# Kernel optimization log

Measured on AMD Instinct MI355X. Metric: run time of the kernel, lower is better.

The kernel has to match this reference:

```python
import math
import jax, jax.numpy as jnp
import numpy as np

HEADS = 8
D_MODEL = 256


def positional_encoding_2d(c, h, w):
    # faithful port of wzlxjtu/PositionalEncoding2D
    d = c // 2
    div_term = jnp.exp(jnp.arange(0.0, d, 2, dtype=jnp.float32) * (-(math.log(10000.0) / d)))  # [d//2? no: d/2 entries -> d//2]
    pos_w = jnp.arange(0.0, w, dtype=jnp.float32)[:, None] * div_term  # [w, d//2]
    pos_h = jnp.arange(0.0, h, dtype=jnp.float32)[:, None] * div_term  # [h, d//2]
    pe = jnp.zeros((c, h, w), dtype=jnp.float32)
    sw = jnp.broadcast_to(jnp.sin(pos_w).T[:, None, :], (div_term.shape[0], h, w))
    cw = jnp.broadcast_to(jnp.cos(pos_w).T[:, None, :], (div_term.shape[0], h, w))
    sh = jnp.broadcast_to(jnp.sin(pos_h).T[:, :, None], (div_term.shape[0], h, w))
    ch = jnp.broadcast_to(jnp.cos(pos_h).T[:, :, None], (div_term.shape[0], h, w))
    pe = pe.at[0:d:2].set(sw)
    pe = pe.at[1:d:2].set(cw)
    pe = pe.at[d::2].set(sh)
    pe = pe.at[d + 1::2].set(ch)
    return pe


def setup_inputs() -> dict:
    key = jax.random.key(0)
    ks = jax.random.split(key, 9)
    b, c, h, w = 2, D_MODEL, 64, 64
    x = jax.random.normal(ks[0], (b, c, h, w), dtype=jnp.float32)
    s = 0.02
    Wq = jax.random.normal(ks[1], (c, c), dtype=jnp.float32) * s
    Wk = jax.random.normal(ks[2], (c, c), dtype=jnp.float32) * s
    Wv = jax.random.normal(ks[3], (c, c), dtype=jnp.float32) * s
    Wo = jax.random.normal(ks[4], (c, c), dtype=jnp.float32) * s
    bq = jax.random.normal(ks[5], (c,), dtype=jnp.float32) * s
    bk = jax.random.normal(ks[6], (c,), dtype=jnp.float32) * s
    bv = jax.random.normal(ks[7], (c,), dtype=jnp.float32) * s
    bo = jax.random.normal(ks[8], (c,), dtype=jnp.float32) * s
    return {"x": x, "Wq": Wq, "bq": bq, "Wk": Wk, "bk": bk,
            "Wv": Wv, "bv": bv, "Wo": Wo, "bo": bo}


def reference(x, Wq, bq, Wk, bk, Wv, bv, Wo, bo):
    b, c, h, w = x.shape
    dk = c // HEADS
    pe = positional_encoding_2d(c, h, w)
    x2 = x + pe[None]                                   # [b,c,h,w]
    tok = x2.reshape(b, c, h * w).transpose(0, 2, 1)    # [b,N,c]
    q = (tok @ Wq.T + bq).reshape(b, -1, HEADS, dk).transpose(0, 2, 1, 3)  # [b,H,N,dk]
    k = (tok @ Wk.T + bk).reshape(b, -1, HEADS, dk).transpose(0, 2, 1, 3)
    v = (tok @ Wv.T + bv).reshape(b, -1, HEADS, dk).transpose(0, 2, 1, 3)
    scores = jnp.einsum('bhnd,bhmd->bhnm', q, k) / math.sqrt(dk)  # [b,H,N,N]
    attn = jax.nn.softmax(scores, axis=-1)
    out = jnp.einsum('bhnm,bhmd->bhnd', attn, v)        # [b,H,N,dk]
    concat = out.transpose(0, 2, 1, 3).reshape(b, -1, c)  # [b,N,c]
    proj = concat @ Wo.T + bo                           # [b,N,c]
    return proj.transpose(0, 2, 1).reshape(b, c, h, w)
```

## Files before the change

kernel.cpp:

```cpp
#include <hip/hip_runtime.h>
#include <hip/hip_bf16.h>
#include <cstdint>

typedef float f32x4 __attribute__((ext_vector_type(4)));
typedef __bf16 bf16x8 __attribute__((ext_vector_type(8)));
typedef uint32_t uint2v __attribute__((ext_vector_type(2)));

#define MFMA_K32(A, B, C) __builtin_amdgcn_mfma_f32_16x16x32_bf16((A), (B), (C), 0, 0, 0)

#if __has_builtin(__builtin_amdgcn_exp2f)
#define EXP2(x) __builtin_amdgcn_exp2f(x)
#else
#define EXP2(x) exp2f(x)
#endif

static __device__ __forceinline__ uint16_t f2b(float f) {
    uint32_t u = __float_as_uint(f);
    uint32_t r = (u + 0x7fffu + ((u >> 16) & 1u)) >> 16;
    return (uint16_t)r;
}

static __device__ __forceinline__ uint32_t packbf(float a, float b) {
    uint32_t r;
    asm("v_cvt_pk_bf16_f32 %0, %1, %2" : "=v"(r) : "v"(a), "v"(b));
    return r;
}

__global__ __launch_bounds__(512) void prep(const float* __restrict__ x,
                                            const float* __restrict__ wq,
                                            const float* __restrict__ wk,
                                            const float* __restrict__ wv,
                                            const float* __restrict__ wo,
                                            uint16_t* __restrict__ dst,
                                            uint16_t* __restrict__ tok) {
    __shared__ uint16_t T[64][65];
    int tid = threadIdx.x, bid = blockIdx.x;
    if (bid < 512) {
        int nt = bid & 63, ct = (bid >> 6) & 3, bb = bid >> 8;
        int n0 = nt << 6, c0 = ct << 6;
        int nl = tid & 63, cq = tid >> 6;
        int n = n0 + nl;
        float pf = (float)((c0 & 128) ? nt : nl);
        int cbase = c0 + cq * 8;
        int ibase = (cbase & 127) >> 1;
        float dt = __expf((float)(2 * ibase) * -0.07195578415606394f);
#pragma unroll
        for (int j = 0; j < 4; ++j) {
            float sv, cv;
            __sincosf(pf * dt, &sv, &cv);
            int cl = cq * 8 + 2 * j;
            int cc = cbase + 2 * j;
            T[cl][nl]     = f2b(x[((size_t)(bb * 256 + cc) << 12) + n] + sv);
            T[cl + 1][nl] = f2b(x[((size_t)(bb * 256 + cc + 1) << 12) + n] + cv);
            dt *= 0.8659643233600653f;
        }
        __syncthreads();
#pragma unroll
        for (int p = 0; p < 8; ++p) {
            int tl = cq * 8 + p;
            tok[(((size_t)(bb << 12) | (n0 + tl)) << 8) + c0 + nl] = T[nl][tl];
        }
    } else {
        int idx = (bid - 512) * 512 + tid;
        int which = idx >> 16, off = idx & 65535;
        const float* s = (which == 0) ? wq : (which == 1) ? wk : (which == 2) ? wv : wo;
        dst[idx] = f2b(s[off]);
    }
}

__global__ __launch_bounds__(256) void qkv_gemm(const uint16_t* __restrict__ tok,
                                                const uint16_t* __restrict__ Wall,
                                                const float* __restrict__ bq,
                                                const float* __restrict__ bk,
                                                const float* __restrict__ bv,
                                                uint16_t* __restrict__ qo,
                                                uint16_t* __restrict__ ko,
                                                uint16_t* __restrict__ vo) {
    __shared__ __align__(16) uint16_t WS[64][264];
    int tid = threadIdx.x, wv = tid >> 6, lane = tid & 63;
    int c16 = lane & 15, quad = lane >> 4;
    int M0 = blockIdx.x * 64 + wv * 16;
    int O0 = blockIdx.y * 64;
    const uint16_t* arow = tok + (size_t)(M0 + c16) * 256;
    bf16x8 af[8];
#pragma unroll
    for (int kk = 0; kk < 8; ++kk) af[kk] = *(const bf16x8*)(arow + kk * 32 + quad * 8);
    f32x4 zero = {0.f, 0.f, 0.f, 0.f};
    int bb = M0 >> 12, n = (M0 + c16) & 4095;
    int srow = tid >> 5, sch = (tid & 31) << 3;
    for (int mat = 0; mat < 3; ++mat) {
        const uint16_t* Wg = Wall + (size_t)mat * 65536 + (size_t)O0 * 256;
        __syncthreads();
#pragma unroll
        for (int p = 0; p < 8; ++p)
            *(bf16x8*)(&WS[p * 8 + srow][sch]) = *(const bf16x8*)(Wg + (p * 8 + srow) * 256 + sch);
        __syncthreads();
        f32x4 acc[4] = {zero, zero, zero, zero};
#pragma unroll
        for (int kk = 0; kk < 8; ++kk) {
            int k0 = kk * 32 + quad * 8;
#pragma unroll
            for (int nb = 0; nb < 4; ++nb)
                acc[nb] = MFMA_K32(*(const bf16x8*)(&WS[nb * 16 + c16][k0]),
                                   af[kk], acc[nb]);
        }
        const float* bias = (mat == 0) ? bq : (mat == 1) ? bk : bv;
        if (mat < 2) {
            float scale = (mat == 0) ? 0.25505654134660127f : 1.0f;
            uint16_t* dst = (mat == 0) ? qo : ko;
#pragma unroll
            for (int nb = 0; nb < 4; ++nb) {
                int o = O0 + nb * 16 + quad * 4;
                f32x4 bi = *(const f32x4*)(bias + o);
                int h = o >> 5, dd = o & 31;
                uint2v pk;
                pk[0] = packbf((acc[nb][0] + bi[0]) * scale, (acc[nb][1] + bi[1]) * scale);
                pk[1] = packbf((acc[nb][2] + bi[2]) * scale, (acc[nb][3] + bi[3]) * scale);
                *(uint2v*)(dst + ((size_t)(bb * 8 + h) * 4096 + n) * 32 + dd) = pk;
            }
        } else {
#pragma unroll
            for (int nb = 0; nb < 4; ++nb)
#pragma unroll
                for (int r = 0; r < 4; ++r) {
                    int o = O0 + nb * 16 + quad * 4 + r;
                    vo[((size_t)(bb * 8 + (o >> 5)) * 32 + (o & 31)) * 4096 + n] =
                        f2b(acc[nb][r] + bias[o]);
                }
        }
    }
}

__global__ __launch_bounds__(512, 8) void flash(const uint16_t* __restrict__ qb,
                                                const uint16_t* __restrict__ kb,
                                                const uint16_t* __restrict__ vtb,
                                                uint16_t* __restrict__ concat) {
    __shared__ __align__(16) char smem[38912];
    int tid = threadIdx.x, wv = tid >> 6, lane = tid & 63;
    int c16 = lane & 15, quad = lane >> 4;
    int half = tid >> 8, t2 = tid & 255;
    int bh = blockIdx.y;
    int q0 = (blockIdx.x << 6) + (wv & 3) * 16;
    size_t base = (size_t)bh << 12;

    uint16_t* KT = (uint16_t*)(smem + half * 19456);
    uint16_t* VT = (uint16_t*)(smem + half * 19456 + 10240);

    const uint16_t* kgp = kb + (base + (size_t)half * 2048 + (t2 >> 2)) * 32 + (t2 & 3) * 8;
    const uint16_t* vgp = vtb + ((size_t)bh * 32 + (t2 >> 3)) * 4096 + half * 2048 + (t2 & 7) * 8;
    uint16_t* kls = KT + (t2 >> 2) * 40 + (t2 & 3) * 8;
    uint16_t* vls = VT + (t2 >> 3) * 72 + (t2 & 7) * 8;

    bf16x8 qf = *(const bf16x8*)(qb + (base + q0 + c16) * 32 + quad * 8);

    int rbase = ((c16 >> 2) << 3) + (c16 & 3);

    union { uint32_t u[4]; bf16x8 v; } onesu;
    onesu.u[0] = 0x3F803F80u; onesu.u[1] = 0x3F803F80u;
    onesu.u[2] = 0x3F803F80u; onesu.u[3] = 0x3F803F80u;
    bf16x8 ones = onesu.v;

    f32x4 zero = {0.f, 0.f, 0.f, 0.f};
    f32x4 oA = zero, oB = zero, oS = zero;

    {
        bf16x8 kr = *(const bf16x8*)kgp;
        bf16x8 vr = *(const bf16x8*)vgp;
        *(bf16x8*)kls = kr;
        *(bf16x8*)vls = vr;
    }
    __syncthreads();

    for (int kt = 0; kt < 32; ++kt) {
        int cur = kt & 1;
        int kn = (kt + 1) & 31;
        bf16x8 kr = *(const bf16x8*)(kgp + (size_t)kn * 2048);
        bf16x8 vr = *(const bf16x8*)(vgp + kn * 64);
        const uint16_t* kfp = KT + cur * 2560 + rbase * 40 + quad * 8;
        const uint16_t* vfp = VT + cur * 2304 + c16 * 72 + quad * 8;
        bf16x8 kf[4], vA[2], vB[2];
        kf[0] = *(const bf16x8*)(kfp);
        kf[1] = *(const bf16x8*)(kfp + 160);
        kf[2] = *(const bf16x8*)(kfp + 1280);
        kf[3] = *(const bf16x8*)(kfp + 1440);
        vA[0] = *(const bf16x8*)(vfp);
        vA[1] = *(const bf16x8*)(vfp + 32);
        vB[0] = *(const bf16x8*)(vfp + 1152);
        vB[1] = *(const bf16x8*)(vfp + 1152 + 32);

        f32x4 s[4];
#pragma unroll
        for (int c = 0; c < 4; ++c) s[c] = MFMA_K32(kf[c], qf, zero);

#pragma unroll
        for (int p = 0; p < 2; ++p) {
#pragma unroll
            for (int r = 0; r < 4; ++r) {
                s[2 * p][r] = EXP2(s[2 * p][r]);
                s[2 * p + 1][r] = EXP2(s[2 * p + 1][r]);
            }
            union { bf16x8 v; uint32_t u[4]; } pa;
            pa.u[0] = packbf(s[2 * p][0], s[2 * p][1]);
            pa.u[1] = packbf(s[2 * p][2], s[2 * p][3]);
            pa.u[2] = packbf(s[2 * p + 1][0], s[2 * p + 1][1]);
            pa.u[3] = packbf(s[2 * p + 1][2], s[2 * p + 1][3]);
            oA = MFMA_K32(pa.v, vA[p], oA);
            oB = MFMA_K32(pa.v, vB[p], oB);
            oS = MFMA_K32(pa.v, ones, oS);
        }

        *(bf16x8*)(kls + (cur ^ 1) * 2560) = kr;
        *(bf16x8*)(vls + (cur ^ 1) * 2304) = vr;
        __syncthreads();
    }

    float* ov = (float*)smem;
    if (wv >= 4) {
        float* d = ov + ((wv - 4) * 64 + lane) * 13;
#pragma unroll
        for (int r = 0; r < 4; ++r) {
            d[r] = oA[r]; d[4 + r] = oB[r]; d[8 + r] = oS[r];
        }
    }
    __syncthreads();
    if (wv < 4) {
        const float* s = ov + (wv * 64 + lane) * 13;
#pragma unroll
        for (int r = 0; r < 4; ++r) {
            oA[r] += s[r]; oB[r] += s[4 + r]; oS[r] += s[8 + r];
        }
        int h = bh & 7, bb = bh >> 3;
#pragma unroll
        for (int r = 0; r < 4; ++r) {
            float i0 = 1.f / oS[r];
            int n = q0 + quad * 4 + r;
            size_t row0 = ((size_t)bb * 4096 + n) * 256 + h * 32;
            concat[row0 + c16]      = f2b(oA[r] * i0);
            concat[row0 + 16 + c16] = f2b(oB[r] * i0);
        }
    }
}

__global__ __launch_bounds__(256) void proj_gemm(const uint16_t* __restrict__ concat,
                                                 const uint16_t* __restrict__ Wo,
                                                 const float* __restrict__ bo,
                                                 float* __restrict__ out) {
    __shared__ __align__(16) uint16_t WS[64][264];
    int tid = threadIdx.x, wv = tid >> 6, lane = tid & 63;
    int c16 = lane & 15, quad = lane >> 4;
    int M0 = blockIdx.x * 64 + wv * 16;
    int O0 = blockIdx.y * 64;
    int srow = tid >> 5, sch = (tid & 31) << 3;
    const uint16_t* Wg = Wo + (size_t)O0 * 256;
#pragma unroll
    for (int p = 0; p < 8; ++p)
        *(bf16x8*)(&WS[p * 8 + srow][sch]) = *(const bf16x8*)(Wg + (p * 8 + srow) * 256 + sch);
    const uint16_t* crow = concat + (size_t)(M0 + c16) * 256;
    bf16x8 af[8];
#pragma unroll
    for (int kk = 0; kk < 8; ++kk) af[kk] = *(const bf16x8*)(crow + kk * 32 + quad * 8);
    __syncthreads();
    f32x4 zero = {0.f, 0.f, 0.f, 0.f};
    f32x4 acc[4] = {zero, zero, zero, zero};
#pragma unroll
    for (int kk = 0; kk < 8; ++kk) {
        int k0 = kk * 32 + quad * 8;
#pragma unroll
        for (int nb = 0; nb < 4; ++nb)
            acc[nb] = MFMA_K32(*(const bf16x8*)(&WS[nb * 16 + c16][k0]),
                               af[kk], acc[nb]);
    }
    int bb = M0 >> 12, n = (M0 + c16) & 4095;
#pragma unroll
    for (int nb = 0; nb < 4; ++nb)
#pragma unroll
        for (int r = 0; r < 4; ++r) {
            int o = O0 + nb * 16 + quad * 4 + r;
            out[((size_t)(bb * 256 + o) << 12) + n] = acc[nb][r] + bo[o];
        }
}

extern "C" void kernel_launch(void* const* d_in, const int* in_sizes, int n_in,
                              void* d_out, int out_size, void* d_ws, size_t ws_size,
                              hipStream_t stream) {
    const float* x  = (const float*)d_in[0];
    const float* Wq = (const float*)d_in[1];
    const float* bq = (const float*)d_in[2];
    const float* Wk = (const float*)d_in[3];
    const float* bk = (const float*)d_in[4];
    const float* Wv = (const float*)d_in[5];
    const float* bv = (const float*)d_in[6];
    const float* Wo = (const float*)d_in[7];
    const float* bo = (const float*)d_in[8];
    float* out = (float*)d_out;

    uint16_t* ws   = (uint16_t*)d_ws;
    uint16_t* Wb   = ws;
    uint16_t* tok  = Wb + 4 * 65536;
    uint16_t* q    = tok + 2097152;
    uint16_t* k    = q + 2097152;
    uint16_t* vt   = k + 2097152;
    uint16_t* cc   = vt + 2097152;

    prep<<<1024, 512, 0, stream>>>(x, Wq, Wk, Wv, Wo, Wb, tok);
    qkv_gemm<<<dim3(128, 4), 256, 0, stream>>>(tok, Wb, bq, bk, bv, q, k, vt);
    flash<<<dim3(64, 16), 512, 0, stream>>>(q, k, vt, cc);
    proj_gemm<<<dim3(128, 4), 256, 0, stream>>>(cc, Wb + 3 * 65536, bo, out);
}
```

Measured before the change: 140.1 us.

## Process four query blocks per wave in flash to reuse K/V tiles

Each wave in the flash kernel now computes 64 query rows instead of 16, holding four Q fragments and four sets of accumulators while iterating over shared K/V tiles. This amortizes K/V global loads, LDS fragment reads and barriers over four times more MFMA work, and the grid shrinks fourfold. The final cross-half reduction is split into two LDS passes to fit the larger accumulator state. The cost is higher register pressure and far fewer resident blocks, which reduces latency hiding through occupancy.

Measured after the change: 144.5 us. 1.03x slower.

```diff
diff --git a/kernel.cpp b/kernel.cpp
--- a/kernel.cpp
+++ b/kernel.cpp
@@ -131,7 +131,7 @@
     }
 }
 
-__global__ __launch_bounds__(512, 8) void flash(const uint16_t* __restrict__ qb,
+__global__ __launch_bounds__(512, 2) void flash(const uint16_t* __restrict__ qb,
                                                 const uint16_t* __restrict__ kb,
                                                 const uint16_t* __restrict__ vtb,
                                                 uint16_t* __restrict__ concat) {
@@ -140,7 +140,7 @@
     int c16 = lane & 15, quad = lane >> 4;
     int half = tid >> 8, t2 = tid & 255;
     int bh = blockIdx.y;
-    int q0 = (blockIdx.x << 6) + (wv & 3) * 16;
+    int q0 = (blockIdx.x << 8) + (wv & 3) * 64;
     size_t base = (size_t)bh << 12;
 
     uint16_t* KT = (uint16_t*)(smem + half * 19456);
@@ -151,7 +151,10 @@
     uint16_t* kls = KT + (t2 >> 2) * 40 + (t2 & 3) * 8;
     uint16_t* vls = VT + (t2 >> 3) * 72 + (t2 & 7) * 8;
 
-    bf16x8 qf = *(const bf16x8*)(qb + (base + q0 + c16) * 32 + quad * 8);
+    bf16x8 qf[4];
+#pragma unroll
+    for (int qbk = 0; qbk < 4; ++qbk)
+        qf[qbk] = *(const bf16x8*)(qb + (base + q0 + qbk * 16 + c16) * 32 + quad * 8);
 
     int rbase = ((c16 >> 2) << 3) + (c16 & 3);
 
@@ -161,7 +164,9 @@
     bf16x8 ones = onesu.v;
 
     f32x4 zero = {0.f, 0.f, 0.f, 0.f};
-    f32x4 oA = zero, oB = zero, oS = zero;
+    f32x4 oA[4], oB[4], oS[4];
+#pragma unroll
+    for (int qbk = 0; qbk < 4; ++qbk) { oA[qbk] = zero; oB[qbk] = zero; oS[qbk] = zero; }
 
     {
         bf16x8 kr = *(const bf16x8*)kgp;
@@ -188,25 +193,27 @@
         vB[0] = *(const bf16x8*)(vfp + 1152);
         vB[1] = *(const bf16x8*)(vfp + 1152 + 32);
 
-        f32x4 s[4];
-#pragma unroll
-        for (int c = 0; c < 4; ++c) s[c] = MFMA_K32(kf[c], qf, zero);
-
-#pragma unroll
-        for (int p = 0; p < 2; ++p) {
-#pragma unroll
-            for (int r = 0; r < 4; ++r) {
-                s[2 * p][r] = EXP2(s[2 * p][r]);
-                s[2 * p + 1][r] = EXP2(s[2 * p + 1][r]);
-            }
-            union { bf16x8 v; uint32_t u[4]; } pa;
-            pa.u[0] = packbf(s[2 * p][0], s[2 * p][1]);
-            pa.u[1] = packbf(s[2 * p][2], s[2 * p][3]);
-            pa.u[2] = packbf(s[2 * p + 1][0], s[2 * p + 1][1]);
-            pa.u[3] = packbf(s[2 * p + 1][2], s[2 * p + 1][3]);
-            oA = MFMA_K32(pa.v, vA[p], oA);
-            oB = MFMA_K32(pa.v, vB[p], oB);
-            oS = MFMA_K32(pa.v, ones, oS);
+#pragma unroll
+        for (int qbk = 0; qbk < 4; ++qbk) {
+            f32x4 s[4];
+#pragma unroll
+            for (int c = 0; c < 4; ++c) s[c] = MFMA_K32(kf[c], qf[qbk], zero);
+#pragma unroll
+            for (int p = 0; p < 2; ++p) {
+#pragma unroll
+                for (int r = 0; r < 4; ++r) {
+                    s[2 * p][r] = EXP2(s[2 * p][r]);
+                    s[2 * p + 1][r] = EXP2(s[2 * p + 1][r]);
+                }
+                union { bf16x8 v; uint32_t u[4]; } pa;
+                pa.u[0] = packbf(s[2 * p][0], s[2 * p][1]);
+                pa.u[1] = packbf(s[2 * p][2], s[2 * p][3]);
+                pa.u[2] = packbf(s[2 * p + 1][0], s[2 * p + 1][1]);
+                pa.u[3] = packbf(s[2 * p + 1][2], s[2 * p + 1][3]);
+                oA[qbk] = MFMA_K32(pa.v, vA[p], oA[qbk]);
+                oB[qbk] = MFMA_K32(pa.v, vB[p], oB[qbk]);
+                oS[qbk] = MFMA_K32(pa.v, ones, oS[qbk]);
+            }
         }
 
         *(bf16x8*)(kls + (cur ^ 1) * 2560) = kr;
@@ -216,28 +223,49 @@
 
     float* ov = (float*)smem;
     if (wv >= 4) {
-        float* d = ov + ((wv - 4) * 64 + lane) * 13;
-#pragma unroll
-        for (int r = 0; r < 4; ++r) {
-            d[r] = oA[r]; d[4 + r] = oB[r]; d[8 + r] = oS[r];
-        }
+        float* d = ov + ((wv - 4) * 64 + lane) * 33;
+#pragma unroll
+        for (int qbk = 0; qbk < 4; ++qbk)
+#pragma unroll
+            for (int r = 0; r < 4; ++r) {
+                d[qbk * 8 + r] = oA[qbk][r];
+                d[qbk * 8 + 4 + r] = oB[qbk][r];
+            }
     }
     __syncthreads();
     if (wv < 4) {
-        const float* s = ov + (wv * 64 + lane) * 13;
-#pragma unroll
-        for (int r = 0; r < 4; ++r) {
-            oA[r] += s[r]; oB[r] += s[4 + r]; oS[r] += s[8 + r];
-        }
+        const float* s = ov + (wv * 64 + lane) * 33;
+#pragma unroll
+        for (int qbk = 0; qbk < 4; ++qbk)
+#pragma unroll
+            for (int r = 0; r < 4; ++r) {
+                oA[qbk][r] += s[qbk * 8 + r];
+                oB[qbk][r] += s[qbk * 8 + 4 + r];
+            }
+    }
+    __syncthreads();
+    if (wv >= 4) {
+        float* d = ov + ((wv - 4) * 64 + lane) * 17;
+#pragma unroll
+        for (int qbk = 0; qbk < 4; ++qbk)
+#pragma unroll
+            for (int r = 0; r < 4; ++r) d[qbk * 4 + r] = oS[qbk][r];
+    }
+    __syncthreads();
+    if (wv < 4) {
+        const float* s = ov + (wv * 64 + lane) * 17;
         int h = bh & 7, bb = bh >> 3;
 #pragma unroll
-        for (int r = 0; r < 4; ++r) {
-            float i0 = 1.f / oS[r];
-            int n = q0 + quad * 4 + r;
-            size_t row0 = ((size_t)bb * 4096 + n) * 256 + h * 32;
-            concat[row0 + c16]      = f2b(oA[r] * i0);
-            concat[row0 + 16 + c16] = f2b(oB[r] * i0);
-        }
+        for (int qbk = 0; qbk < 4; ++qbk)
+#pragma unroll
+            for (int r = 0; r < 4; ++r) {
+                float l = oS[qbk][r] + s[qbk * 4 + r];
+                float inv = 1.f / l;
+                int n = q0 + qbk * 16 + quad * 4 + r;
+                size_t row = ((size_t)bb * 4096 + n) * 256 + h * 32;
+                concat[row + c16]      = f2b(oA[qbk][r] * inv);
+                concat[row + 16 + c16] = f2b(oB[qbk][r] * inv);
+            }
     }
 }
 
@@ -304,6 +332,6 @@
 
     prep<<<1024, 512, 0, stream>>>(x, Wq, Wk, Wv, Wo, Wb, tok);
     qkv_gemm<<<dim3(128, 4), 256, 0, stream>>>(tok, Wb, bq, bk, bv, q, k, vt);
-    flash<<<dim3(64, 16), 512, 0, stream>>>(q, k, vt, cc);
+    flash<<<dim3(16, 16), 512, 0, stream>>>(q, k, vt, cc);
     proj_gemm<<<dim3(128, 4), 256, 0, stream>>>(cc, Wb + 3 * 65536, bo, out);
 }
```
